# Kernel optimization log

Measured on AMD Instinct MI355X. Metric: run time of the kernel, lower is better.

## Reference

```python
import jax, jax.numpy as jnp
import numpy as np

D_MODEL = 256
D_IN = (D_MODEL + 1) ** 2  # 66049


def setup_inputs() -> dict:
    key = jax.random.key(0)
    k1, k2, k3, k4 = jax.random.split(key, 4)
    X = jax.random.normal(k1, (16, 256, 256), dtype=jnp.float32)
    X_aux = jax.random.normal(k2, (16, 256, 256), dtype=jnp.float32)
    # nn.Linear params: weight [out, in], bias [out]
    W = jax.random.normal(k3, (D_MODEL, D_IN), dtype=jnp.float32) / np.sqrt(D_IN)
    b = jax.random.normal(k4, (D_MODEL,), dtype=jnp.float32) * 0.01
    return {"X": X, "X_aux": X_aux, "W": W, "b": b}


def reference(X, X_aux, W, b):
    bsz, t, d = X.shape
    ones = jnp.ones((bsz, t, 1), dtype=X.dtype)
    Xa = jnp.concatenate([ones, X], axis=2)        # [b, t, d+1]
    Xb = jnp.concatenate([ones, X_aux], axis=2)    # [b, t, d+1]
    # outer product per (b, t): [b, t, d+1, d+1]
    tf = jnp.einsum("bti,btj->btij", Xa, Xb)
    tf = tf.reshape(bsz, t, -1)                    # [b, t, (d+1)^2]
    out = jnp.einsum("btk,ok->bto", tf, W) + b     # [b, t, d_model]
    return out
```

## Files before the change

kernel.cpp:

```cpp
#include <hip/hip_runtime.h>
#include <hip/hip_bf16.h>


#define DI 66049

typedef __attribute__((ext_vector_type(8))) short bf16x8;
typedef __attribute__((ext_vector_type(4))) float f32x4;

__device__ __forceinline__ unsigned short f2b(float f) {
  union { __hip_bfloat16 h; unsigned short u; } cv;
  cv.h = __float2bfloat16(f);
  return cv.u;
}

__device__ __forceinline__ bf16x8 pack8(f32x4 lo, f32x4 hi) {
  bf16x8 r;
  r[0] = (short)f2b(lo[0]); r[1] = (short)f2b(lo[1]);
  r[2] = (short)f2b(lo[2]); r[3] = (short)f2b(lo[3]);
  r[4] = (short)f2b(hi[0]); r[5] = (short)f2b(hi[1]);
  r[6] = (short)f2b(hi[2]); r[7] = (short)f2b(hi[3]);
  return r;
}

__device__ __forceinline__ void gload16(const void* g, void* l) {
  __builtin_amdgcn_global_load_lds(
      (const __attribute__((address_space(1))) unsigned int*)g,
      (__attribute__((address_space(3))) unsigned int*)l, 16, 0, 0);
}

__global__ void prep_w(const float* __restrict__ W, unsigned short* __restrict__ Bp) {
  const int c = blockIdx.x;
  const int o = (blockIdx.y << 2) + (threadIdx.x >> 6);
  const int j = (threadIdx.x & 63) << 2;
  const float* wrow = W + (size_t)o * DI;
  float v0, v1, v2, v3;
  if (c < 256) {
    const int bse = (c + 1) * 257 + 1 + j;
    v0 = wrow[bse]; v1 = wrow[bse + 1]; v2 = wrow[bse + 2]; v3 = wrow[bse + 3];
  } else if (c == 256) {
    const int bse = 1 + j;
    v0 = wrow[bse]; v1 = wrow[bse + 1]; v2 = wrow[bse + 2]; v3 = wrow[bse + 3];
  } else {
    v0 = wrow[(j + 1) * 257]; v1 = wrow[(j + 2) * 257];
    v2 = wrow[(j + 3) * 257]; v3 = wrow[(j + 4) * 257];
  }
  unsigned short* dst = Bp + (((size_t)c << 8) + o) * 256 + j;
  const unsigned int lo = (unsigned int)f2b(v0) | ((unsigned int)f2b(v1) << 16);
  const unsigned int hi = (unsigned int)f2b(v2) | ((unsigned int)f2b(v3) << 16);
  *(uint2*)dst = make_uint2(lo, hi);
}

__global__ void prep_xt(const float* __restrict__ X, float* __restrict__ Xt) {
  __shared__ float t[32][33];
  const int tx = threadIdx.x, ty = threadIdx.y;
  const int bt0 = blockIdx.x << 5, c0 = blockIdx.y << 5;
#pragma unroll
  for (int k = 0; k < 4; ++k) {
    const int row = (ty << 2) + k;
    t[row][tx] = X[(size_t)(bt0 + row) * 256 + c0 + tx];
  }
  __syncthreads();
#pragma unroll
  for (int k = 0; k < 4; ++k) {
    const int row = (ty << 2) + k;
    Xt[(size_t)(c0 + row) * 4096 + bt0 + tx] = t[tx][row];
  }
}

#define PACK_AS(SRC)                                                           \
  {                                                                            \
    const int _row = tid >> 2, _q = tid & 3;                                   \
    const float* _rp = (SRC) + (size_t)(bt0 + _row) * 256 + (_q << 6);         \
    const int _sx = _row & 15;                                                 \
    _Pragma("unroll") for (int _w = 0; _w < 8; ++_w) {                         \
      f32x4 _lo = *(const f32x4*)(_rp + (_w << 3));                            \
      f32x4 _hi = *(const f32x4*)(_rp + (_w << 3) + 4);                        \
      const int _slot = (_q << 3) + _w;                                        \
      *(bf16x8*)(&As[_row * 256 + ((_slot ^ _sx) << 3)]) = pack8(_lo, _hi);    \
    }                                                                          \
  }

#define STAGE(C, JB, BUF)                                                      \
  {                                                                            \
    const unsigned _cb = ((unsigned)(C) << 16) + (unsigned)(JB);               \
    _Pragma("unroll") for (int _e = 0; _e < 4; ++_e) {                         \
      gload16(Bp + _cb + stg_off[_e],                                          \
              &Bs[BUF][(size_t)(((_e << 9) | tid)) << 3]);                     \
    }                                                                          \
  }

#define NEXT_CJ(K4, CN, JBN)                                                   \
  int _nk = (ci << 2) + (K4) + 1;                                              \
  if (_nk > nkmax) _nk = nkmax;                                                \
  const int _nci = _nk >> 2;                                                   \
  const int CN = is7 ? (_nci < 32 ? 225 + _nci : 257) : c0 + _nci;             \
  const int JBN = (_nk & 3) << 6;

#define KT(K4, CUR, EXTRA)                                                     \
  {                                                                            \
    NEXT_CJ(K4, _cn, _jbn);                                                    \
    STAGE(_cn, _jbn, (CUR) ^ 1);                                               \
    asm volatile("s_waitcnt vmcnt(4)" ::: "memory");                           \
    __builtin_amdgcn_s_barrier();                                              \
    bf16x8 bf0[4], bf1[4];                                                     \
    _Pragma("unroll") for (int fn = 0; fn < 4; ++fn) {                         \
      const int _rb = (wn << 6) + (fn << 4) + l15;                             \
      const int _rx = _rb & 7;                                                 \
      bf0[fn] = *(const bf16x8*)(&Bs[CUR][_rb * 64 + ((lg ^ _rx) << 3)]);      \
      bf1[fn] = *(const bf16x8*)(&Bs[CUR][_rb * 64 + (((4 + lg) ^ _rx) << 3)]);\
    }                                                                          \
    bf16x8 _aA[4], _aB[4];                                                     \
    _Pragma("unroll") for (int rg = 0; rg < 4; ++rg) {                         \
      const int _ra = wr + (rg << 4) + l15;                                    \
      const int _sx = _ra & 15;                                                \
      _aA[rg] = *(const bf16x8*)(&As[_ra * 256 +                               \
                                     (((((K4) << 3) + lg) ^ _sx) << 3)]);      \
      _aB[rg] = *(const bf16x8*)(&As[_ra * 256 +                               \
                                     (((((K4) << 3) + 4 + lg) ^ _sx) << 3)]);  \
    }                                                                          \
    EXTRA;                                                                     \
    __builtin_amdgcn_s_setprio(1);                                             \
    _Pragma("unroll") for (int rg = 0; rg < 4; ++rg)                           \
      _Pragma("unroll") for (int fn = 0; fn < 4; ++fn) {                       \
        t[rg][fn] = __builtin_amdgcn_mfma_f32_16x16x32_bf16(                   \
            _aA[rg], bf0[fn], t[rg][fn], 0, 0, 0);                             \
        t[rg][fn] = __builtin_amdgcn_mfma_f32_16x16x32_bf16(                   \
            _aB[rg], bf1[fn], t[rg][fn], 0, 0, 0);                             \
      }                                                                        \
    __builtin_amdgcn_s_setprio(0);                                             \
    __builtin_amdgcn_s_barrier();                                              \
  }

__global__ __launch_bounds__(512, 1) void gemm_r9(
    const float* __restrict__ X, const float* __restrict__ Xb,
    const float* __restrict__ Xt, const unsigned short* __restrict__ Bp,
    float* __restrict__ P) {
  __shared__ __align__(16) unsigned short As[128 * 256];
  __shared__ __align__(16) unsigned short Bs[2][256 * 64];
  __shared__ __align__(16) float Ss[33 * 128];

  const int tid = threadIdx.x;
  const int rid = blockIdx.x;
  const int slice = rid & 7;
  const int bx = rid >> 3;
  const int bt0 = bx << 7;
  const bool is7 = (slice == 7);
  const int c0 = is7 ? 225 : slice * 32 + (slice ? 1 : 0);
  const int nCh = (slice == 0 || is7) ? 33 : 32;
  const int nkmax = (nCh << 2) - 1;

  const int wid = tid >> 6, lane = tid & 63;
  const int wm = wid >> 2, wn = wid & 3;
  const int wr = wm << 6;
  const int l15 = lane & 15, lg = lane >> 4;

  unsigned stg_off[4];
#pragma unroll
  for (int e = 0; e < 4; ++e) {
    const int row = (e << 6) | (tid >> 3);
    const int sl = (tid & 7) ^ (row & 7);
    stg_off[e] = (unsigned)(row * 256 + (sl << 3));
  }

  PACK_AS(Xb);
  for (int i = tid; i < (nCh << 7); i += 512) {
    const int ci = i >> 7, r = i & 127;
    const int c = is7 ? (ci < 32 ? 225 + ci : 257) : c0 + ci;
    Ss[i] = (c < 256) ? Xt[(size_t)c * 4096 + bt0 + r] : 1.0f;
  }
  STAGE(c0, 0, 0);
  __syncthreads();

  f32x4 acc[4][4] = {};

  for (int ci = 0; ci < nCh; ++ci) {
    f32x4 t[4][4] = {};
    f32x4 s4[4];
    KT(0, 0, {});
    KT(1, 1, {});
    KT(2, 0, {});
    KT(3, 1, {
      _Pragma("unroll") for (int rg = 0; rg < 4; ++rg)
          s4[rg] = *(const f32x4*)(&Ss[(ci << 7) + wr + (rg << 4) + (lg << 2)]);
    });
#pragma unroll
    for (int rg = 0; rg < 4; ++rg)
#pragma unroll
      for (int fn = 0; fn < 4; ++fn) acc[rg][fn] += s4[rg] * t[rg][fn];

    if (is7 && ci == 31) {
      __syncthreads();
      PACK_AS(X);
      __syncthreads();
    }
  }

  float* pp = P + ((size_t)slice << 20);
#pragma unroll
  for (int rg = 0; rg < 4; ++rg) {
    const int row = bt0 + wr + (rg << 4) + (lg << 2);
#pragma unroll
    for (int fn = 0; fn < 4; ++fn) {
      const int col = (wn << 6) + (fn << 4) + l15;
#pragma unroll
      for (int e = 0; e < 4; ++e)
        pp[(size_t)(row + e) * 256 + col] = acc[rg][fn][e];
    }
  }
}

__global__ void reduce_k(const float* __restrict__ P, const float* __restrict__ W,
                         const float* __restrict__ b, float* __restrict__ out,
                         int nsl) {
  const int idx = blockIdx.x * 256 + threadIdx.x;
  const int o = idx & 255;
  float v = b[o] + W[(size_t)o * DI];
  for (int s = 0; s < nsl; ++s) v += P[idx + (size_t)s * 1048576];
  out[idx] = v;
}

__global__ void init_k(const float* __restrict__ W, const float* __restrict__ b,
                       float* __restrict__ out) {
  const int idx = blockIdx.x * 256 + threadIdx.x;
  const int o = idx & 255;
  out[idx] = b[o] + W[(size_t)o * DI];
}

__global__ __launch_bounds__(256, 4) void gemm_fb(
    const float* __restrict__ X, const float* __restrict__ Xa,
    const float* __restrict__ W, float* __restrict__ Out) {
  __shared__ __align__(16) unsigned short Asf[128 * 64];
  __shared__ __align__(16) unsigned short Bsf[128 * 64];
  const int tid = threadIdx.x;
  const int bx = blockIdx.x, by = blockIdx.y, bz = blockIdx.z;
  const int S = gridDim.z;
  const int bt0 = bx << 7, o0 = by << 7;
  const int q = 258 / S, r = 258 % S;
  const int c0 = bz * q + (bz < r ? bz : r);
  const int ccnt = q + (bz < r ? 1 : 0);
  const int nK = ccnt << 2;
  const int wid = tid >> 6, lane = tid & 63;
  const int wr = (wid >> 1) << 6, wc = (wid & 1) << 6;
  const int ar = tid >> 1;
  const int ah = (tid & 1) << 5;
  const float* xrow = X + (size_t)(bt0 + ar) * 256;
  const float* varow = Xa + (size_t)(bt0 + ar) * 256;
  f32x4 acc[4][4] = {};
  for (int kt = 0; kt < nK; ++kt) {
    const int c = c0 + (kt >> 2);
    const int j0 = (kt & 3) << 6;
    __syncthreads();
    {
      const float* vs = (c == 257) ? xrow : varow;
      float s = 1.0f;
      if (c < 256) s = xrow[c];
      const f32x4* vp = (const f32x4*)(vs + j0 + ah);
      f32x4 v[8];
#pragma unroll
      for (int qq = 0; qq < 8; ++qq) v[qq] = vp[qq];
      unsigned short* aw = Asf + ar * 64;
      const int sl0 = ah >> 3, sx = ar & 7;
#pragma unroll
      for (int w = 0; w < 4; ++w) {
        bf16x8 pk;
#pragma unroll
        for (int e = 0; e < 8; ++e)
          pk[e] = (short)f2b(s * v[w * 2 + (e >> 2)][e & 3]);
        *(bf16x8*)(aw + (((sl0 + w) ^ sx) << 3)) = pk;
      }
    }
    {
      const int orow = tid >> 1;
      const int jh = (tid & 1) << 5;
      const float* wrow = W + (size_t)(o0 + orow) * DI;
      float tmp[32];
      if (c < 256) {
        const int bse = (c + 1) * 257 + 1 + j0 + jh;
#pragma unroll
        for (int i = 0; i < 32; ++i) tmp[i] = wrow[bse + i];
      } else if (c == 256) {
        const int bse = 1 + j0 + jh;
#pragma unroll
        for (int i = 0; i < 32; ++i) tmp[i] = wrow[bse + i];
      } else {
#pragma unroll
        for (int i = 0; i < 32; ++i) tmp[i] = wrow[(j0 + jh + i + 1) * 257];
      }
      unsigned short* bw = Bsf + orow * 64;
      const int sl0 = jh >> 3, sx = orow & 7;
#pragma unroll
      for (int w = 0; w < 4; ++w) {
        bf16x8 pk;
#pragma unroll
        for (int e = 0; e < 8; ++e) pk[e] = (short)f2b(tmp[w * 8 + e]);
        *(bf16x8*)(bw + (((sl0 + w) ^ sx) << 3)) = pk;
      }
    }
    __syncthreads();
#pragma unroll
    for (int kk = 0; kk < 2; ++kk) {
      const int kslot = (kk << 2) + (lane >> 4);
      bf16x8 af[4], bfr2[4];
#pragma unroll
      for (int fm = 0; fm < 4; ++fm) {
        const int row = wr + (fm << 4) + (lane & 15);
        af[fm] = *(const bf16x8*)(Asf + row * 64 + ((kslot ^ (row & 7)) << 3));
      }
#pragma unroll
      for (int fn = 0; fn < 4; ++fn) {
        const int row = wc + (fn << 4) + (lane & 15);
        bfr2[fn] = *(const bf16x8*)(Bsf + row * 64 + ((kslot ^ (row & 7)) << 3));
      }
#pragma unroll
      for (int fm = 0; fm < 4; ++fm)
#pragma unroll
        for (int fn = 0; fn < 4; ++fn)
          acc[fm][fn] = __builtin_amdgcn_mfma_f32_16x16x32_bf16(
              af[fm], bfr2[fn], acc[fm][fn], 0, 0, 0);
    }
  }
  const int r0 = (lane >> 4) << 2;
  const int cl = lane & 15;
#pragma unroll
  for (int fm = 0; fm < 4; ++fm) {
    const int row = bt0 + wr + (fm << 4) + r0;
#pragma unroll
    for (int fn = 0; fn < 4; ++fn) {
      const int col = o0 + wc + (fn << 4) + cl;
#pragma unroll
      for (int rr = 0; rr < 4; ++rr)
        atomicAdd(Out + (size_t)(row + rr) * 256 + col, acc[fm][fn][rr]);
    }
  }
}

extern "C" void kernel_launch(void* const* d_in, const int* in_sizes, int n_in,
                              void* d_out, int out_size, void* d_ws, size_t ws_size,
                              hipStream_t stream) {
  const float* X  = (const float*)d_in[0];
  const float* Xa = (const float*)d_in[1];
  const float* W  = (const float*)d_in[2];
  const float* b  = (const float*)d_in[3];
  float* out = (float*)d_out;

  const size_t WBF_SZ = (size_t)258 * 256 * 256 * 2;
  const size_t XT_SZ  = (size_t)256 * 4096 * 4;
  const size_t PART1  = (size_t)4096 * 256 * 4;

  if (ws_size >= WBF_SZ + XT_SZ + 8 * PART1) {
    unsigned short* Bp = (unsigned short*)d_ws;
    float* Xt = (float*)((char*)d_ws + WBF_SZ);
    float* P  = (float*)((char*)d_ws + WBF_SZ + XT_SZ);
    prep_w<<<dim3(258, 64), 256, 0, stream>>>(W, Bp);
    prep_xt<<<dim3(128, 8), dim3(32, 8), 0, stream>>>(X, Xt);
    gemm_r9<<<dim3(256), 512, 0, stream>>>(X, Xa, Xt, Bp, P);
    reduce_k<<<4096, 256, 0, stream>>>(P, W, b, out, 8);
  } else {
    init_k<<<4096, 256, 0, stream>>>(W, b, out);
    gemm_fb<<<dim3(32, 2, 4), 256, 0, stream>>>(X, Xa, W, out);
  }
}
```

Before: 183.8 us.

## Deepen B staging to 4-buffer ring with register fragment prefetch, split chunk-257 work

Restructures the GEMM main loop to use a four-slot ring of smaller (32-wide K) B tiles staged three steps ahead, and double-buffers A/B fragments in registers so LDS reads for the next step overlap the current MFMAs. Removes the per-step trailing barrier and the mid-loop re-pack of A in slice 7 by moving the X-side chunk 257 into 32 extra blocks writing a ninth partial slice, with reduce summing nine slices. This trades more blocks, more workspace and one more partial to reduce for a shallower dependency between global loads and MFMA issue. It also evens out per-block chunk counts.

```diff
diff --git a/kernel.cpp b/kernel.cpp
--- a/kernel.cpp
+++ b/kernel.cpp
@@ -80,122 +80,130 @@
     }                                                                          \
   }
 
-#define STAGE(C, JB, BUF)                                                      \
+#define STAGE_U(V, SLOT)                                                       \
   {                                                                            \
-    const unsigned _cb = ((unsigned)(C) << 16) + (unsigned)(JB);               \
-    _Pragma("unroll") for (int _e = 0; _e < 4; ++_e) {                         \
-      gload16(Bp + _cb + stg_off[_e],                                          \
-              &Bs[BUF][(size_t)(((_e << 9) | tid)) << 3]);                     \
+    const unsigned short* _bse =                                               \
+        Bp + ((size_t)(c0 + ((V) >> 3)) << 16) + (((V) & 7) << 5);             \
+    gload16(_bse + stg_off0, &Bs[SLOT][(size_t)tid << 3]);                     \
+    gload16(_bse + stg_off1, &Bs[SLOT][(size_t)(512 + tid) << 3]);             \
+  }
+
+#define READ_FRAGS(U, S)                                                       \
+  {                                                                            \
+    const int _uh4 = ((U) & 7) << 2;                                           \
+    _Pragma("unroll") for (int _rg = 0; _rg < 4; ++_rg) {                      \
+      const int _ra = wr + (_rg << 4) + l15;                                   \
+      fa[S][_rg] = *(const bf16x8*)(&As[_ra * 256 +                            \
+                                        (((_uh4 + lg) ^ (_ra & 15)) << 3)]);   \
     }                                                                          \
-  }
-
-#define NEXT_CJ(K4, CN, JBN)                                                   \
-  int _nk = (ci << 2) + (K4) + 1;                                              \
-  if (_nk > nkmax) _nk = nkmax;                                                \
-  const int _nci = _nk >> 2;                                                   \
-  const int CN = is7 ? (_nci < 32 ? 225 + _nci : 257) : c0 + _nci;             \
-  const int JBN = (_nk & 3) << 6;
-
-#define KT(K4, CUR, EXTRA)                                                     \
-  {                                                                            \
-    NEXT_CJ(K4, _cn, _jbn);                                                    \
-    STAGE(_cn, _jbn, (CUR) ^ 1);                                               \
-    asm volatile("s_waitcnt vmcnt(4)" ::: "memory");                           \
-    __builtin_amdgcn_s_barrier();                                              \
-    bf16x8 bf0[4], bf1[4];                                                     \
-    _Pragma("unroll") for (int fn = 0; fn < 4; ++fn) {                         \
-      const int _rb = (wn << 6) + (fn << 4) + l15;                             \
-      const int _rx = _rb & 7;                                                 \
-      bf0[fn] = *(const bf16x8*)(&Bs[CUR][_rb * 64 + ((lg ^ _rx) << 3)]);      \
-      bf1[fn] = *(const bf16x8*)(&Bs[CUR][_rb * 64 + (((4 + lg) ^ _rx) << 3)]);\
+    _Pragma("unroll") for (int _fn = 0; _fn < 4; ++_fn) {                      \
+      const int _rb = (wn << 6) + (_fn << 4) + l15;                            \
+      fb[S][_fn] = *(const bf16x8*)(&Bs[(U) & 3][_rb * 32 +                    \
+                                        ((lg ^ ((_rb >> 1) & 3)) << 3)]);      \
     }                                                                          \
-    bf16x8 _aA[4], _aB[4];                                                     \
-    _Pragma("unroll") for (int rg = 0; rg < 4; ++rg) {                         \
-      const int _ra = wr + (rg << 4) + l15;                                    \
-      const int _sx = _ra & 15;                                                \
-      _aA[rg] = *(const bf16x8*)(&As[_ra * 256 +                               \
-                                     (((((K4) << 3) + lg) ^ _sx) << 3)]);      \
-      _aB[rg] = *(const bf16x8*)(&As[_ra * 256 +                               \
-                                     (((((K4) << 3) + 4 + lg) ^ _sx) << 3)]);  \
-    }                                                                          \
-    EXTRA;                                                                     \
-    __builtin_amdgcn_s_setprio(1);                                             \
-    _Pragma("unroll") for (int rg = 0; rg < 4; ++rg)                           \
-      _Pragma("unroll") for (int fn = 0; fn < 4; ++fn) {                       \
-        t[rg][fn] = __builtin_amdgcn_mfma_f32_16x16x32_bf16(                   \
-            _aA[rg], bf0[fn], t[rg][fn], 0, 0, 0);                             \
-        t[rg][fn] = __builtin_amdgcn_mfma_f32_16x16x32_bf16(                   \
-            _aB[rg], bf1[fn], t[rg][fn], 0, 0, 0);                             \
-      }                                                                        \
-    __builtin_amdgcn_s_setprio(0);                                             \
-    __builtin_amdgcn_s_barrier();                                              \
-  }
-
-__global__ __launch_bounds__(512, 1) void gemm_r9(
+  }
+
+__global__ __launch_bounds__(512, 1) void gemm_r10(
     const float* __restrict__ X, const float* __restrict__ Xb,
     const float* __restrict__ Xt, const unsigned short* __restrict__ Bp,
     float* __restrict__ P) {
   __shared__ __align__(16) unsigned short As[128 * 256];
-  __shared__ __align__(16) unsigned short Bs[2][256 * 64];
+  __shared__ __align__(16) unsigned short Bs[4][256 * 32];
   __shared__ __align__(16) float Ss[33 * 128];
 
   const int tid = threadIdx.x;
   const int rid = blockIdx.x;
-  const int slice = rid & 7;
-  const int bx = rid >> 3;
+
+  int bx, c0, nCh, Pslice;
+  const float* Asrc;
+  if (rid < 256) {
+    const int slice = rid & 7;
+    bx = rid >> 3;
+    c0 = slice << 5;
+    nCh = (slice == 7) ? 33 : 32;
+    Asrc = Xb;
+    Pslice = slice;
+  } else {
+    bx = rid - 256;
+    c0 = 257;
+    nCh = 1;
+    Asrc = X;
+    Pslice = 8;
+  }
   const int bt0 = bx << 7;
-  const bool is7 = (slice == 7);
-  const int c0 = is7 ? 225 : slice * 32 + (slice ? 1 : 0);
-  const int nCh = (slice == 0 || is7) ? 33 : 32;
-  const int nkmax = (nCh << 2) - 1;
+  const int nU = nCh << 3;
 
   const int wid = tid >> 6, lane = tid & 63;
   const int wm = wid >> 2, wn = wid & 3;
   const int wr = wm << 6;
   const int l15 = lane & 15, lg = lane >> 4;
 
-  unsigned stg_off[4];
-#pragma unroll
-  for (int e = 0; e < 4; ++e) {
-    const int row = (e << 6) | (tid >> 3);
-    const int sl = (tid & 7) ^ (row & 7);
-    stg_off[e] = (unsigned)(row * 256 + (sl << 3));
-  }
-
-  PACK_AS(Xb);
+  const int idx0 = tid, idx1 = 512 + tid;
+  const int row0 = idx0 >> 2, row1 = idx1 >> 2;
+  const unsigned stg_off0 =
+      (unsigned)(row0 * 256 + (((idx0 & 3) ^ ((row0 >> 1) & 3)) << 3));
+  const unsigned stg_off1 =
+      (unsigned)(row1 * 256 + (((idx1 & 3) ^ ((row1 >> 1) & 3)) << 3));
+
+  PACK_AS(Asrc);
   for (int i = tid; i < (nCh << 7); i += 512) {
-    const int ci = i >> 7, r = i & 127;
-    const int c = is7 ? (ci < 32 ? 225 + ci : 257) : c0 + ci;
+    const int ci2 = i >> 7, r = i & 127;
+    const int c = c0 + ci2;
     Ss[i] = (c < 256) ? Xt[(size_t)c * 4096 + bt0 + r] : 1.0f;
   }
-  STAGE(c0, 0, 0);
+  STAGE_U(0, 0);
+  STAGE_U(1, 1);
+  STAGE_U(2, 2);
   __syncthreads();
+
+  bf16x8 fa[2][4], fb[2][4];
+  READ_FRAGS(0, 0);
 
   f32x4 acc[4][4] = {};
 
   for (int ci = 0; ci < nCh; ++ci) {
     f32x4 t[4][4] = {};
     f32x4 s4[4];
-    KT(0, 0, {});
-    KT(1, 1, {});
-    KT(2, 0, {});
-    KT(3, 1, {
-      _Pragma("unroll") for (int rg = 0; rg < 4; ++rg)
-          s4[rg] = *(const f32x4*)(&Ss[(ci << 7) + wr + (rg << 4) + (lg << 2)]);
-    });
+#pragma unroll
+    for (int uh = 0; uh < 8; ++uh) {
+      const int u = (ci << 3) + uh;
+      int v = u + 3;
+      if (v > nU - 1) v = nU - 1;
+      STAGE_U(v, (u + 3) & 3);
+      asm volatile("s_waitcnt vmcnt(4)" ::: "memory");
+      __builtin_amdgcn_s_barrier();
+      int un = u + 1;
+      if (un > nU - 1) un = nU - 1;
+      if (uh & 1) {
+        READ_FRAGS(un, 0);
+      } else {
+        READ_FRAGS(un, 1);
+      }
+      if (uh == 7) {
+#pragma unroll
+        for (int rg = 0; rg < 4; ++rg)
+          s4[rg] =
+              *(const f32x4*)(&Ss[(ci << 7) + wr + (rg << 4) + (lg << 2)]);
+      }
+      __builtin_amdgcn_s_setprio(1);
+#pragma unroll
+      for (int rg = 0; rg < 4; ++rg)
+#pragma unroll
+        for (int fn = 0; fn < 4; ++fn)
+          t[rg][fn] = (uh & 1)
+                          ? __builtin_amdgcn_mfma_f32_16x16x32_bf16(
+                                fa[1][rg], fb[1][fn], t[rg][fn], 0, 0, 0)
+                          : __builtin_amdgcn_mfma_f32_16x16x32_bf16(
+                                fa[0][rg], fb[0][fn], t[rg][fn], 0, 0, 0);
+      __builtin_amdgcn_s_setprio(0);
+    }
 #pragma unroll
     for (int rg = 0; rg < 4; ++rg)
 #pragma unroll
       for (int fn = 0; fn < 4; ++fn) acc[rg][fn] += s4[rg] * t[rg][fn];
-
-    if (is7 && ci == 31) {
-      __syncthreads();
-      PACK_AS(X);
-      __syncthreads();
-    }
-  }
-
-  float* pp = P + ((size_t)slice << 20);
+  }
+
+  float* pp = P + ((size_t)Pslice << 20);
 #pragma unroll
   for (int rg = 0; rg < 4; ++rg) {
     const int row = bt0 + wr + (rg << 4) + (lg << 2);
@@ -347,14 +355,14 @@
   const size_t XT_SZ  = (size_t)256 * 4096 * 4;
   const size_t PART1  = (size_t)4096 * 256 * 4;
 
-  if (ws_size >= WBF_SZ + XT_SZ + 8 * PART1) {
+  if (ws_size >= WBF_SZ + XT_SZ + 9 * PART1) {
     unsigned short* Bp = (unsigned short*)d_ws;
     float* Xt = (float*)((char*)d_ws + WBF_SZ);
     float* P  = (float*)((char*)d_ws + WBF_SZ + XT_SZ);
     prep_w<<<dim3(258, 64), 256, 0, stream>>>(W, Bp);
     prep_xt<<<dim3(128, 8), dim3(32, 8), 0, stream>>>(X, Xt);
-    gemm_r9<<<dim3(256), 512, 0, stream>>>(X, Xa, Xt, Bp, P);
-    reduce_k<<<4096, 256, 0, stream>>>(P, W, b, out, 8);
+    gemm_r10<<<dim3(288), 512, 0, stream>>>(X, Xa, Xt, Bp, P);
+    reduce_k<<<4096, 256, 0, stream>>>(P, W, b, out, 9);
   } else {
     init_k<<<4096, 256, 0, stream>>>(W, b, out);
     gemm_fb<<<dim3(32, 2, 4), 256, 0, stream>>>(X, Xa, W, out);
```

Measured after the change: 174.3 us. 5.2% less time.
